# Kernel optimization log

Hardware: AMD Instinct MI355X
Metric: run time of the kernel (lower is better)

## Reference

```python
import jax, jax.numpy as jnp
import numpy as np

AMBIENT = [2, 2, 2]
DEGREES = [a + 1 for a in AMBIENT]          # coords per projective factor
N_COORDS = sum(DEGREES)                      # 9
STARTS = np.concatenate([[0], np.cumsum(DEGREES)[:-1]])
CONST_MULT = 1.0
CLIP = 1.0e6


def _get_real_imag_of_prod(cp):
    """cp: complex [B, n]. Returns (real [B, n(n+1)/2], imag [B, n(n-1)/2]).
    Matches TF boolean_mask(transpose(...)) ordering: row-major (b, a) with b<=a;
    real = (XX+YY)[x, b, a] (symmetric), imag = +XY_YX[x, b, a] for b<a."""
    X, Y = jnp.real(cp), jnp.imag(cp)
    XX_YY = jnp.einsum('xa,xb->xab', X, X) + jnp.einsum('xa,xb->xab', Y, Y)
    XY = jnp.einsum('xa,xb->xab', X, Y)
    XY_YX = XY - XY.transpose(0, 2, 1)      # antisymmetric
    n = cp.shape[1]
    iu = jnp.triu_indices(n)                # incl. diagonal
    su = jnp.triu_indices(n, 1)             # strict upper
    real = XX_YY[:, iu[0], iu[1]]
    imag = XY_YX[:, su[0], su[1]]
    return real, imag


def _bihom(points):
    """points: complex [B, N_COORDS] -> real [B, 729] section products / kappa."""
    B = points.shape[0]
    kappas_prod = jnp.ones((B,), points.real.dtype)
    it_r = it_i = None
    for i, (s, d) in enumerate(zip(STARTS, DEGREES)):
        cp = points[:, s:s + d]
        kappas_prod = kappas_prod * jnp.sum(jnp.abs(cp) ** 2, axis=-1)
        r, im = _get_real_imag_of_prod(cp)
        if i == 0:
            it_r, it_i = r, im
        else:
            new_r = jnp.concatenate([
                jnp.einsum('bi,bj->bij', it_r, r).reshape(B, -1),
                -jnp.einsum('bi,bj->bij', it_i, im).reshape(B, -1)], axis=1)
            new_i = jnp.concatenate([
                jnp.einsum('bi,bj->bij', it_r, im).reshape(B, -1),
                -jnp.einsum('bi,bj->bij', it_i, r).reshape(B, -1)], axis=1)
            it_r, it_i = new_r, new_i
    sec = jnp.concatenate([it_r, it_i], axis=-1)
    return sec / kappas_prod[:, None]


def _tower(h, W1, b1, W2, b2, W3, b3, Wf):
    # Dense layers with square activation, then log|.| into bias-free final Dense
    h = (h @ W1 + b1) ** 2
    h = (h @ W2 + b2) ** 2
    h = (h @ W3 + b3) ** 2
    return jnp.log(jnp.abs(h)) @ Wf


def setup_inputs() -> dict:
    key = jax.random.key(0)
    ks = jax.random.split(key, 16)
    B = 32768
    s = 0.05
    inp = {
        'x':   jax.random.normal(ks[0], (B, 2 * N_COORDS), jnp.float32),
        'W1a': jax.random.normal(ks[1], (729, 1024), jnp.float32) * s,
        'b1a': jax.random.normal(ks[2], (1024,), jnp.float32) * s,
        'W2a': jax.random.normal(ks[3], (1024, 1024), jnp.float32) * s,
        'b2a': jax.random.normal(ks[4], (1024,), jnp.float32) * s,
        'W3a': jax.random.normal(ks[5], (1024, 1), jnp.float32) * s,
        'b3a': jax.random.normal(ks[6], (1,), jnp.float32) * s,
        'Wfa': jnp.ones((1, 1), jnp.float32),
        'W1b': jax.random.normal(ks[7], (729, 1024), jnp.float32) * s,
        'b1b': jax.random.normal(ks[8], (1024,), jnp.float32) * s,
        'W2b': jax.random.normal(ks[9], (1024, 1024), jnp.float32) * s,
        'b2b': jax.random.normal(ks[10], (1024,), jnp.float32) * s,
        'W3b': jax.random.normal(ks[11], (1024, 1), jnp.float32) * s,
        'b3b': jax.random.normal(ks[12], (1,), jnp.float32) * s,
        'Wfb': jnp.ones((1, 1), jnp.float32),
    }
    return inp


def reference(x, W1a, b1a, W2a, b2a, W3a, b3a, Wfa,
              W1b, b1b, W2b, b2b, W3b, b3b, Wfb):
    points = jax.lax.complex(x[:, :N_COORDS], x[:, N_COORDS:])
    feats = _bihom(points)                     # [B, 729]
    out = _tower(feats, W1a, b1a, W2a, b2a, W3a, b3a, Wfa) \
        - _tower(feats, W1b, b1b, W2b, b2b, W3b, b3b, Wfb)
    return CONST_MULT * jnp.clip(out, -CLIP, CLIP)
```

## Files before the change

kernel.cpp:

```cpp
#include <hip/hip_runtime.h>

typedef unsigned short u16;
typedef unsigned int u32;
typedef __attribute__((ext_vector_type(8))) short bf16x8;
typedef __attribute__((ext_vector_type(4))) float f32x4;

__device__ __forceinline__ u16 f2bf(float x){
  unsigned u = __builtin_bit_cast(unsigned, x);
  unsigned r = (u + 0x7FFFu + ((u >> 16) & 1u)) >> 16;
  return (u16)r;
}
__device__ __forceinline__ float bf2f(u16 h){
  unsigned u = ((unsigned)h) << 16;
  return __builtin_bit_cast(float, u);
}

__device__ __forceinline__ void gld_lds16(const void* g, void* l){
  __builtin_amdgcn_global_load_lds((const __attribute__((address_space(1))) void*)g,
                                   (__attribute__((address_space(3))) void*)l,
                                   16, 0, 0);
}

__global__ void wconv_kernel(const float* __restrict__ W0, u16* __restrict__ Th0, int K0p,
                             const float* __restrict__ W1, u16* __restrict__ Th1, int K1p,
                             const float* __restrict__ W2, u16* __restrict__ Th2, int K2p,
                             const float* __restrict__ W3, u16* __restrict__ Th3, int K3p)
{
  __shared__ float t[32][33];
  int z = blockIdx.z;
  const float* W = z==0 ? W0 : z==1 ? W1 : z==2 ? W2 : W3;
  u16* Th = z==0 ? Th0 : z==1 ? Th1 : z==2 ? Th2 : Th3;
  int Kpad = z==0 ? K0p : z==1 ? K1p : z==2 ? K2p : K3p;
  int K = (Kpad == 768) ? 729 : 1024;
  int k0 = blockIdx.x * 32;
  if (k0 >= Kpad) return;
  int n0 = blockIdx.y * 32;
  int tx = threadIdx.x & 31, ty = threadIdx.x >> 5;
#pragma unroll
  for (int j = 0; j < 4; j++){
    int k = k0 + ty + j*8;
    float v = (k < K) ? W[(size_t)k*1024 + (n0 + tx)] : 0.f;
    t[ty + j*8][tx] = v;
  }
  __syncthreads();
#pragma unroll
  for (int j = 0; j < 4; j++){
    int n = n0 + ty + j*8;
    int k = k0 + tx;
    size_t idx = (size_t)n*Kpad + k;
    Th[idx] = f2bf(t[tx][ty + j*8]);
  }
}

__global__ void feats_kernel(const float* __restrict__ x,
                             u16* __restrict__ fh,
                             int row0)
{
  __shared__ float cC[8][28];
  __shared__ float tA[8][81];
  __shared__ float tB[8][12];
  __shared__ float ivk[8];
  const int tid = threadIdx.x;
  const int lrow0 = blockIdx.x * 8;
  if (tid < 8){
    const float* xr = x + (size_t)(row0 + lrow0 + tid) * 18;
    float kk = 1.f;
#pragma unroll
    for (int f = 0; f < 3; f++){
      float xa = xr[3*f+0], xb = xr[3*f+1], xc = xr[3*f+2];
      float ya = xr[9+3*f+0], yb = xr[9+3*f+1], yc = xr[9+3*f+2];
      int bse = f * 9;
      cC[tid][bse+0] = xa*xa + ya*ya;
      cC[tid][bse+1] = xa*xb + ya*yb;
      cC[tid][bse+2] = xa*xc + ya*yc;
      cC[tid][bse+3] = xb*xb + yb*yb;
      cC[tid][bse+4] = xb*xc + yb*yc;
      cC[tid][bse+5] = xc*xc + yc*yc;
      cC[tid][bse+6] = xa*yb - xb*ya;
      cC[tid][bse+7] = xa*yc - xc*ya;
      cC[tid][bse+8] = xb*yc - xc*yb;
      kk *= (xa*xa+ya*ya + xb*xb+yb*yb + xc*xc+yc*yc);
    }
    ivk[tid] = 1.f / kk;
#pragma unroll
    for (int j = 0; j < 6; j++) tB[tid][j] = cC[tid][18+j];
#pragma unroll
    for (int j = 0; j < 3; j++) tB[tid][6+j] = cC[tid][24+j];
  }
  __syncthreads();
#pragma unroll 1
  for (int e = tid; e < 648; e += 256){
    int r = e / 81;
    int k = e - r*81;
    const float* cc = cC[r];
    float val;
    if (k < 36)      {               val =   cc[k/6]     * cc[9  + k%6]; }
    else if (k < 45) { int u = k-36; val = -(cc[6 + u/3] * cc[15 + u%3]); }
    else if (k < 63) { int u = k-45; val =   cc[u/3]     * cc[15 + u%3]; }
    else             { int u = k-63; val = -(cc[6 + u/6] * cc[9  + u%6]); }
    tA[r][k] = val;
  }
  __syncthreads();
#pragma unroll 1
  for (int jj = 0; jj < 3; jj++){
    int o = jj*256 + tid;
    int idxA = 0, idxB = 0; float sgn = 0.f;
    if (o < 270)      {              idxA = o/6;      idxB = o - (o/6)*6; sgn =  1.f; }
    else if (o < 378) { int t = o-270; idxA = 45 + t/3; idxB = 6 + t%3;   sgn = -1.f; }
    else if (o < 513) { int t = o-378; idxA = t/3;      idxB = 6 + t%3;   sgn =  1.f; }
    else if (o < 729) { int t = o-513; idxA = 45 + t/6; idxB = t%6;       sgn = -1.f; }
#pragma unroll
    for (int r = 0; r < 8; r++){
      float v = sgn * tA[r][idxA] * tB[r][idxB] * ivk[r];
      size_t oi = (size_t)(lrow0 + r) * 768 + o;
      fh[oi] = f2bf(v);
    }
  }
}

#define GEMM_SMEM_BYTES 65536

#define STAGE_A(BUF)  do{ u16* _a = sA + (BUF)*8192; \
    gld_lds16(gAh0, _a + wave*1024); gld_lds16(gAh1, _a + wave*1024 + 512); \
    gAh0 += 32; gAh1 += 32; }while(0)
#define STAGE_B(BUF) do{ u16* _b = sB + (BUF)*8192; \
    gld_lds16(gBh0, _b + wave*1024); gld_lds16(gBh1, _b + wave*1024 + 512); \
    gBh0 += 32; gBh1 += 32; }while(0)

#define BARRIER()  asm volatile("s_barrier" ::: "memory")
#define LGKM0()    asm volatile("s_waitcnt lgkmcnt(0)" ::: "memory")

#define CLUSTER(A, O, B) do{ \
    __builtin_amdgcn_s_setprio(1); \
    _Pragma("unroll") for (int m_ = 0; m_ < 4; m_++) \
      _Pragma("unroll") for (int n_ = 0; n_ < 4; n_++) \
        acc[(O)+m_][n_] = __builtin_amdgcn_mfma_f32_16x16x32_bf16((A)[m_], (B)[n_], acc[(O)+m_][n_], 0, 0, 0); \
    __builtin_amdgcn_s_setprio(0); \
  }while(0)

template<int MODE>
__global__ __launch_bounds__(512, 1) void gemm_k(
    const u16* __restrict__ Ahi,
    const u16* __restrict__ Bhi,
    const float* __restrict__ bias,
    u16* __restrict__ Oh,
    const float* __restrict__ W3, float* __restrict__ P, int Pstride,
    int K)
{
  extern __shared__ __align__(16) u16 smem[];
  u16* sA = smem;
  u16* sB = smem + 16384;
  float* rowsum = (float*)smem;

  const int nwg = gridDim.x;
  const int qq = nwg >> 3;
  const int wg = (nwg & 7) ? (int)blockIdx.x
                           : ((blockIdx.x & 7) * qq + (blockIdx.x >> 3));
  const int nb = wg & 3;
  const int mb = wg >> 2;

  const int tid = threadIdx.x;
  const int wave = tid >> 6, lane = tid & 63;
  const int wm = wave >> 2, wn = wave & 3;

  const int l4 = lane >> 2, ls = lane & 3;
  const int fsw  = (l4 >> 1) & 3;
  const int koff = ((ls ^ fsw) << 3);

  const u16* gAh0 = Ahi + (size_t)(mb*256 + wave*32 + l4) * K + koff;
  const u16* gAh1 = gAh0 + (size_t)16 * K;
  const u16* gBh0 = Bhi + (size_t)(nb*256 + wave*32 + l4) * K + koff;
  const u16* gBh1 = gBh0 + (size_t)16 * K;

  const int r16 = lane & 15, g = lane >> 4;
  const int fr   = (r16 >> 1) & 3;
  const int slot = ((g ^ fr) << 3);

  f32x4 acc[8][4];
#pragma unroll
  for (int m = 0; m < 8; m++)
#pragma unroll
    for (int n = 0; n < 4; n++)
      acc[m][n] = (f32x4){0.f, 0.f, 0.f, 0.f};

  const int NT = K >> 5;
  STAGE_A(0); STAGE_B(0);
  asm volatile("s_waitcnt vmcnt(0)\n\ts_barrier" ::: "memory");

#pragma unroll 1
  for (int t = 0; t < NT; ++t){
    const int cur = t & 1, nxt = cur ^ 1;
    const u16* pA = sA + cur*8192;
    const u16* pB = sB + cur*8192;
    const bool pf = (t + 1 < NT);
    bf16x8 ah[8], bh[4];

#pragma unroll
    for (int n = 0; n < 4; n++) bh[n] = *(const bf16x8*)(pB + (wn*64 + n*16 + r16)*32 + slot);
#pragma unroll
    for (int m = 0; m < 4; m++) ah[m] = *(const bf16x8*)(pA + (wm*128 + m*16 + r16)*32 + slot);
    if (pf){ STAGE_A(nxt); }
    BARRIER(); LGKM0();
    CLUSTER(ah, 0, bh);
    BARRIER();

#pragma unroll
    for (int m = 0; m < 4; m++) ah[4+m] = *(const bf16x8*)(pA + (wm*128 + (4+m)*16 + r16)*32 + slot);
    if (pf){ STAGE_B(nxt); }
    BARRIER(); LGKM0();
    CLUSTER(ah+4, 4, bh);
    if (pf){
      asm volatile("s_waitcnt vmcnt(0)\n\ts_barrier" ::: "memory");
    } else {
      BARRIER();
    }
  }

  if constexpr (MODE == 0){
#pragma unroll
    for (int n = 0; n < 4; n++){
      int col = nb*256 + wn*64 + n*16 + r16;
      float bv = bias[col];
#pragma unroll
      for (int m = 0; m < 8; m++){
        int rbase = mb*256 + wm*128 + m*16 + g*4;
#pragma unroll
        for (int q = 0; q < 4; q++){
          float val = acc[m][n][q] + bv;
          val = val * val;
          size_t oi = (size_t)(rbase + q) * 1024 + col;
          Oh[oi] = f2bf(val);
        }
      }
    }
  } else {
    float w3v[4], bv[4];
#pragma unroll
    for (int n = 0; n < 4; n++){
      int col = nb*256 + wn*64 + n*16 + r16;
      w3v[n] = W3[col];
      bv[n]  = bias[col];
    }
    float rp[8][4];
#pragma unroll
    for (int m = 0; m < 8; m++)
#pragma unroll
      for (int q = 0; q < 4; q++)
        rp[m][q] = 0.f;
#pragma unroll
    for (int m = 0; m < 8; m++)
#pragma unroll
      for (int n = 0; n < 4; n++)
#pragma unroll
        for (int q = 0; q < 4; q++){
          float v = acc[m][n][q] + bv[n];
          rp[m][q] += v * v * w3v[n];
        }
#pragma unroll
    for (int m = 0; m < 8; m++)
#pragma unroll
      for (int q = 0; q < 4; q++){
        float s = rp[m][q];
        s += __shfl_xor(s, 1); s += __shfl_xor(s, 2);
        s += __shfl_xor(s, 4); s += __shfl_xor(s, 8);
        rp[m][q] = s;
      }
    __syncthreads();
    if (r16 == 0){
#pragma unroll
      for (int m = 0; m < 8; m++)
#pragma unroll
        for (int q = 0; q < 4; q++)
          rowsum[wn*256 + wm*128 + m*16 + g*4 + q] = rp[m][q];
    }
    __syncthreads();
    if (tid < 256){
      float s = rowsum[tid] + rowsum[256 + tid] + rowsum[512 + tid] + rowsum[768 + tid];
      P[(size_t)nb * Pstride + mb*256 + tid] = s;
    }
  }
}

__global__ void finalize_kernel(const float* __restrict__ Pa, const float* __restrict__ Pb,
                                int Pstride,
                                const float* __restrict__ b3a, const float* __restrict__ Wfa,
                                const float* __restrict__ b3b, const float* __restrict__ Wfb,
                                float* __restrict__ out, int row0, int Rc)
{
  int r = blockIdx.x * 256 + threadIdx.x;
  if (r >= Rc) return;
  float sa = b3a[0], sb = b3b[0];
#pragma unroll
  for (int j = 0; j < 4; j++){
    sa += Pa[(size_t)j * Pstride + r];
    sb += Pb[(size_t)j * Pstride + r];
  }
  float ta = 2.f * logf(fabsf(sa)) * Wfa[0];
  float tb = 2.f * logf(fabsf(sb)) * Wfb[0];
  float o = ta - tb;
  o = fminf(fmaxf(o, -1000000.f), 1000000.f);
  out[row0 + r] = o;
}

static inline size_t align256(size_t v){ return (v + 255) & ~(size_t)255; }

extern "C" void kernel_launch(void* const* d_in, const int* in_sizes, int n_in,
                              void* d_out, int out_size, void* d_ws, size_t ws_size,
                              hipStream_t stream)
{
  (void)n_in; (void)out_size;
  const float* x   = (const float*)d_in[0];
  const float* W1a = (const float*)d_in[1];
  const float* b1a = (const float*)d_in[2];
  const float* W2a = (const float*)d_in[3];
  const float* b2a = (const float*)d_in[4];
  const float* W3a = (const float*)d_in[5];
  const float* b3a = (const float*)d_in[6];
  const float* Wfa = (const float*)d_in[7];
  const float* W1b = (const float*)d_in[8];
  const float* b1b = (const float*)d_in[9];
  const float* W2b = (const float*)d_in[10];
  const float* b2b = (const float*)d_in[11];
  const float* W3b = (const float*)d_in[12];
  const float* b3b = (const float*)d_in[13];
  const float* Wfb = (const float*)d_in[14];
  float* out = (float*)d_out;

  const int B  = in_sizes[0] / 18;
  const int K1 = 768;
  const int K2 = 1024;

  char* base = (char*)d_ws;
  size_t off = 0;
  auto carve = [&](size_t bytes) -> char* {
    off = align256(off);
    char* p = base + off;
    off += bytes;
    return p;
  };

  u16* wt1a = (u16*)carve((size_t)1024 * K1 * 2);
  u16* wt2a = (u16*)carve((size_t)1024 * K2 * 2);
  u16* wt1b = (u16*)carve((size_t)1024 * K1 * 2);
  u16* wt2b = (u16*)carve((size_t)1024 * K2 * 2);

  size_t fixed = align256(off);
  const long long per_row = (long long)K1*2 + 2048 + 32;
  long long avail = (long long)ws_size - (long long)fixed - 8192;
  long long rmax = avail > 0 ? avail / per_row : 0;
  int R = (int)((rmax / 256) * 256);
  if (R > B) R = B;
  if (R < 256) R = 256;

  u16* fh  = (u16*)carve((size_t)R * K1 * 2);
  u16* h1h = (u16*)carve((size_t)R * 1024 * 2);
  float* pa = (float*)carve((size_t)4 * R * 4);
  float* pb = (float*)carve((size_t)4 * R * 4);

  wconv_kernel<<<dim3(32, 32, 4), 256, 0, stream>>>(
      W1a, wt1a, K1,
      W2a, wt2a, K2,
      W1b, wt1b, K1,
      W2b, wt2b, K2);

  for (int row0 = 0; row0 < B; row0 += R){
    int Rc = B - row0; if (Rc > R) Rc = R;
    int MB = Rc / 256;
    feats_kernel<<<Rc/8, 256, 0, stream>>>(x, fh, row0);
    gemm_k<0><<<dim3(4*MB), 512, GEMM_SMEM_BYTES, stream>>>(
        fh, wt1a, b1a, h1h, nullptr, nullptr, 0, K1);
    gemm_k<1><<<dim3(4*MB), 512, GEMM_SMEM_BYTES, stream>>>(
        h1h, wt2a, b2a, nullptr, W3a, pa, R, K2);
    gemm_k<0><<<dim3(4*MB), 512, GEMM_SMEM_BYTES, stream>>>(
        fh, wt1b, b1b, h1h, nullptr, nullptr, 0, K1);
    gemm_k<1><<<dim3(4*MB), 512, GEMM_SMEM_BYTES, stream>>>(
        h1h, wt2b, b2b, nullptr, W3b, pb, R, K2);
    finalize_kernel<<<(Rc + 255)/256, 256, 0, stream>>>(pa, pb, R, b3a, Wfa, b3b, Wfb,
                                                        out, row0, Rc);
  }
}
```

Before: 310.0 us.

## Shrink GEMM tile to 256x128 with 4 waves per block

The GEMM workgroup tile changes from 256x256 with 8 waves to 256x128 with 4 waves. Each wave now covers 128x64 of output, the B staging buffer is halved, and LDS use drops to about 50KB. This doubles the grid and the number of partial row-sum slices in the fused second layer, so finalize now reduces 8 partials instead of 4. The aim is more workgroups for better CU fill, and possibly two blocks per CU, in exchange for reloading the A tile across twice as many N blocks.

```diff
diff --git a/kernel.cpp b/kernel.cpp
--- a/kernel.cpp
+++ b/kernel.cpp
@@ -118,14 +118,15 @@
   }
 }
 
-#define GEMM_SMEM_BYTES 65536
-
-#define STAGE_A(BUF)  do{ u16* _a = sA + (BUF)*8192; \
-    gld_lds16(gAh0, _a + wave*1024); gld_lds16(gAh1, _a + wave*1024 + 512); \
-    gAh0 += 32; gAh1 += 32; }while(0)
-#define STAGE_B(BUF) do{ u16* _b = sB + (BUF)*8192; \
-    gld_lds16(gBh0, _b + wave*1024); gld_lds16(gBh1, _b + wave*1024 + 512); \
-    gBh0 += 32; gBh1 += 32; }while(0)
+#define GEMM_SMEM_BYTES (32768 + 16384 + 2048)
+
+#define STAGE_A(BUF)  do{ u16* _a = sA + (BUF)*8192 + wave*2048; \
+    gld_lds16(gA0, _a);        gld_lds16(gA1, _a + 512); \
+    gld_lds16(gA2, _a + 1024); gld_lds16(gA3, _a + 1536); \
+    gA0 += 32; gA1 += 32; gA2 += 32; gA3 += 32; }while(0)
+#define STAGE_B(BUF) do{ u16* _b = sB + (BUF)*4096 + wave*1024; \
+    gld_lds16(gB0, _b); gld_lds16(gB1, _b + 512); \
+    gB0 += 32; gB1 += 32; }while(0)
 
 #define BARRIER()  asm volatile("s_barrier" ::: "memory")
 #define LGKM0()    asm volatile("s_waitcnt lgkmcnt(0)" ::: "memory")
@@ -139,7 +140,7 @@
   }while(0)
 
 template<int MODE>
-__global__ __launch_bounds__(512, 1) void gemm_k(
+__global__ __launch_bounds__(256, 1) void gemm_k(
     const u16* __restrict__ Ahi,
     const u16* __restrict__ Bhi,
     const float* __restrict__ bias,
@@ -150,27 +151,29 @@
   extern __shared__ __align__(16) u16 smem[];
   u16* sA = smem;
   u16* sB = smem + 16384;
-  float* rowsum = (float*)smem;
+  float* rowsum = (float*)(smem + 24576);
 
   const int nwg = gridDim.x;
   const int qq = nwg >> 3;
   const int wg = (nwg & 7) ? (int)blockIdx.x
                            : ((blockIdx.x & 7) * qq + (blockIdx.x >> 3));
-  const int nb = wg & 3;
-  const int mb = wg >> 2;
+  const int nb = wg & 7;
+  const int mb = wg >> 3;
 
   const int tid = threadIdx.x;
   const int wave = tid >> 6, lane = tid & 63;
-  const int wm = wave >> 2, wn = wave & 3;
+  const int wm = wave >> 1, wn = wave & 1;
 
   const int l4 = lane >> 2, ls = lane & 3;
   const int fsw  = (l4 >> 1) & 3;
   const int koff = ((ls ^ fsw) << 3);
 
-  const u16* gAh0 = Ahi + (size_t)(mb*256 + wave*32 + l4) * K + koff;
-  const u16* gAh1 = gAh0 + (size_t)16 * K;
-  const u16* gBh0 = Bhi + (size_t)(nb*256 + wave*32 + l4) * K + koff;
-  const u16* gBh1 = gBh0 + (size_t)16 * K;
+  const u16* gA0 = Ahi + (size_t)(mb*256 + wave*64 + l4) * K + koff;
+  const u16* gA1 = gA0 + (size_t)16 * K;
+  const u16* gA2 = gA0 + (size_t)32 * K;
+  const u16* gA3 = gA0 + (size_t)48 * K;
+  const u16* gB0 = Bhi + (size_t)(nb*128 + wave*32 + l4) * K + koff;
+  const u16* gB1 = gB0 + (size_t)16 * K;
 
   const int r16 = lane & 15, g = lane >> 4;
   const int fr   = (r16 >> 1) & 3;
@@ -191,7 +194,7 @@
   for (int t = 0; t < NT; ++t){
     const int cur = t & 1, nxt = cur ^ 1;
     const u16* pA = sA + cur*8192;
-    const u16* pB = sB + cur*8192;
+    const u16* pB = sB + cur*4096;
     const bool pf = (t + 1 < NT);
     bf16x8 ah[8], bh[4];
 
@@ -219,7 +222,7 @@
   if constexpr (MODE == 0){
 #pragma unroll
     for (int n = 0; n < 4; n++){
-      int col = nb*256 + wn*64 + n*16 + r16;
+      int col = nb*128 + wn*64 + n*16 + r16;
       float bv = bias[col];
 #pragma unroll
       for (int m = 0; m < 8; m++){
@@ -237,7 +240,7 @@
     float w3v[4], bv[4];
 #pragma unroll
     for (int n = 0; n < 4; n++){
-      int col = nb*256 + wn*64 + n*16 + r16;
+      int col = nb*128 + wn*64 + n*16 + r16;
       w3v[n] = W3[col];
       bv[n]  = bias[col];
     }
@@ -265,7 +268,6 @@
         s += __shfl_xor(s, 4); s += __shfl_xor(s, 8);
         rp[m][q] = s;
       }
-    __syncthreads();
     if (r16 == 0){
 #pragma unroll
       for (int m = 0; m < 8; m++)
@@ -275,7 +277,7 @@
     }
     __syncthreads();
     if (tid < 256){
-      float s = rowsum[tid] + rowsum[256 + tid] + rowsum[512 + tid] + rowsum[768 + tid];
+      float s = rowsum[tid] + rowsum[256 + tid];
       P[(size_t)nb * Pstride + mb*256 + tid] = s;
     }
   }
@@ -291,7 +293,7 @@
   if (r >= Rc) return;
   float sa = b3a[0], sb = b3b[0];
 #pragma unroll
-  for (int j = 0; j < 4; j++){
+  for (int j = 0; j < 8; j++){
     sa += Pa[(size_t)j * Pstride + r];
     sb += Pb[(size_t)j * Pstride + r];
   }
@@ -345,7 +347,7 @@
   u16* wt2b = (u16*)carve((size_t)1024 * K2 * 2);
 
   size_t fixed = align256(off);
-  const long long per_row = (long long)K1*2 + 2048 + 32;
+  const long long per_row = (long long)K1*2 + 2048 + 64;
   long long avail = (long long)ws_size - (long long)fixed - 8192;
   long long rmax = avail > 0 ? avail / per_row : 0;
   int R = (int)((rmax / 256) * 256);
@@ -354,8 +356,8 @@
 
   u16* fh  = (u16*)carve((size_t)R * K1 * 2);
   u16* h1h = (u16*)carve((size_t)R * 1024 * 2);
-  float* pa = (float*)carve((size_t)4 * R * 4);
-  float* pb = (float*)carve((size_t)4 * R * 4);
+  float* pa = (float*)carve((size_t)8 * R * 4);
+  float* pb = (float*)carve((size_t)8 * R * 4);
 
   wconv_kernel<<<dim3(32, 32, 4), 256, 0, stream>>>(
       W1a, wt1a, K1,
@@ -367,13 +369,13 @@
     int Rc = B - row0; if (Rc > R) Rc = R;
     int MB = Rc / 256;
     feats_kernel<<<Rc/8, 256, 0, stream>>>(x, fh, row0);
-    gemm_k<0><<<dim3(4*MB), 512, GEMM_SMEM_BYTES, stream>>>(
+    gemm_k<0><<<dim3(8*MB), 256, GEMM_SMEM_BYTES, stream>>>(
         fh, wt1a, b1a, h1h, nullptr, nullptr, 0, K1);
-    gemm_k<1><<<dim3(4*MB), 512, GEMM_SMEM_BYTES, stream>>>(
+    gemm_k<1><<<dim3(8*MB), 256, GEMM_SMEM_BYTES, stream>>>(
         h1h, wt2a, b2a, nullptr, W3a, pa, R, K2);
-    gemm_k<0><<<dim3(4*MB), 512, GEMM_SMEM_BYTES, stream>>>(
+    gemm_k<0><<<dim3(8*MB), 256, GEMM_SMEM_BYTES, stream>>>(
         fh, wt1b, b1b, h1h, nullptr, nullptr, 0, K1);
-    gemm_k<1><<<dim3(4*MB), 512, GEMM_SMEM_BYTES, stream>>>(
+    gemm_k<1><<<dim3(8*MB), 256, GEMM_SMEM_BYTES, stream>>>(
         h1h, wt2b, b2b, nullptr, W3b, pb, R, K2);
     finalize_kernel<<<(Rc + 255)/256, 256, 0, stream>>>(pa, pb, R, b3a, Wfa, b3b, Wfb,
                                                         out, row0, Rc);
```

Result: slower. 387.5 us (+25.0%).
